# Kernel tuning notes

Measured on AMD Instinct MI355X. Metric: run time of the kernel, lower is better.

The kernel has to match this reference:

```python
import jax, jax.numpy as jnp
import numpy as np

N_NODES = 32768
NUM_EDGES = 524288
NUM_GRAPHS = 32
C = 128            # hidden channels
N_LAYERS = 3       # len(hidden_channels)-1
D_IN = 144         # 4 (op embedding dim) + 140
C_MID = 80         # mem1 out
C_OUT = 64         # mem2 out / classes
H1, K1N = 5, 10    # mem1 heads / clusters
H2, K2N = 5, 1     # mem2 heads / clusters
EPS = 1e-15


def _gatv2(x, src, dst, Wl, bl, Wr, br, att, cb):
    """GATv2Conv (heads=1, negative_slope=0.2), edges src->dst incl. self loops."""
    n = x.shape[0]
    xl = x @ Wl + bl                                  # source transform [N,C]
    xr = x @ Wr + br                                  # target transform [N,C]
    e = (jax.nn.leaky_relu(xl[src] + xr[dst], 0.2) @ att)  # [E]
    m = jax.ops.segment_max(e, dst, num_segments=n)   # segment softmax over in-edges
    ee = jnp.exp(e - m[dst])
    denom = jax.ops.segment_sum(ee, dst, num_segments=n)
    alpha = ee / denom[dst]
    out = jax.ops.segment_sum(alpha[:, None] * xl[src], dst, num_segments=n)
    return out + cb


def _bn(h, gamma, beta):
    # BatchNorm1d with batch statistics (training-mode forward), eps=1e-5
    mu = h.mean(0)
    var = h.var(0)
    return (h - mu) * jax.lax.rsqrt(var + 1e-5) * gamma + beta


def _mem_pool(xd, Kmem, W):
    # xd [B,N,C], Kmem [H,K,C]; Student-t kernel, tau=1 -> (1+d)^-1
    d = (jnp.sum(xd * xd, -1)[:, :, None, None]
         + jnp.sum(Kmem * Kmem, -1)[None, None]
         - 2.0 * jnp.einsum('bnc,hkc->bnhk', xd, Kmem))  # [B,N,H,K] sq. distances
    S = 1.0 / (1.0 + d)
    S = S / S.sum(-1, keepdims=True)   # normalize over clusters
    S = S.mean(2)                      # average heads -> [B,N,K]
    out = jnp.einsum('bnk,bnc->bkc', S, xd) @ W
    return out, S


def _kl_loss(S):
    S2 = S * S / S.sum(1, keepdims=True)
    den = S2.sum(2, keepdims=True)
    den = jnp.where(S.sum(2, keepdims=True) == 0.0, 1.0, den)
    P = jnp.maximum(S2 / den, EPS)
    Sc = jnp.maximum(S, EPS)
    # KLDivLoss(reduction='batchmean'), input = log(S)
    return jnp.sum(P * (jnp.log(P) - jnp.log(Sc))) / S.shape[0]


def setup_inputs():
    key = jax.random.key(0)
    ks = jax.random.split(key, 24)
    x = jax.random.normal(ks[0], (N_NODES, D_IN), jnp.float32)
    edge_index = jax.random.randint(ks[1], (2, NUM_EDGES), 0, N_NODES, jnp.int32)
    batch = (jnp.arange(N_NODES, dtype=jnp.int32) // (N_NODES // NUM_GRAPHS))
    s = 1.0 / np.sqrt(C)
    inp = {
        'x': x, 'edge_index': edge_index, 'batch': batch,
        'W_in': jax.random.normal(ks[2], (D_IN, C), jnp.float32) / np.sqrt(D_IN),
        'b_in': jnp.zeros((C,), jnp.float32),
        'bn_gamma': jnp.ones((N_LAYERS, C), jnp.float32),
        'bn_beta': jnp.zeros((N_LAYERS, C), jnp.float32),
        'Wl': jax.random.normal(ks[3], (N_LAYERS, C, C), jnp.float32) * s,
        'bl': jnp.zeros((N_LAYERS, C), jnp.float32),
        'Wr': jax.random.normal(ks[4], (N_LAYERS, C, C), jnp.float32) * s,
        'br': jnp.zeros((N_LAYERS, C), jnp.float32),
        'att': jax.random.normal(ks[5], (N_LAYERS, C), jnp.float32) * s,
        'conv_bias': jnp.zeros((N_LAYERS, C), jnp.float32),
        'K1': jax.random.normal(ks[6], (H1, K1N, C), jnp.float32),
        'Wm1': jax.random.normal(ks[7], (C, C_MID), jnp.float32) * s,
        'K2': jax.random.normal(ks[8], (H2, K2N, C_MID), jnp.float32),
        'Wm2': jax.random.normal(ks[9], (C_MID, C_OUT), jnp.float32) / np.sqrt(C_MID),
    }
    return inp


def reference(x, edge_index, batch, W_in, b_in, bn_gamma, bn_beta,
              Wl, bl, Wr, br, att, conv_bias, K1, Wm1, K2, Wm2):
    h = x @ W_in + b_in                               # self.linear
    loops = jnp.arange(N_NODES, dtype=edge_index.dtype)
    src = jnp.concatenate([edge_index[0], loops])     # GATv2 add_self_loops=True
    dst = jnp.concatenate([edge_index[1], loops])
    for l in range(N_LAYERS):                         # DeepGCNLayer block='res+'
        t = _bn(h, bn_gamma[l], bn_beta[l])
        t = jax.nn.leaky_relu(t, 0.01)
        # dropout: identity (deterministic reference)
        t = _gatv2(t, src, dst, Wl[l], bl[l], Wr[l], br[l], att[l], conv_bias[l])
        h = h + t
    per = N_NODES // NUM_GRAPHS
    xd = h.reshape(NUM_GRAPHS, per, C)                # to_dense_batch (equal-size graphs)
    x1, S1 = _mem_pool(xd, K1, Wm1)                   # [B,10,80]
    x1 = jax.nn.leaky_relu(x1, 0.01)
    x2, S2 = _mem_pool(x1, K2, Wm2)                   # [B,1,64]
    logits = jax.nn.log_softmax(x2.squeeze(1), -1)    # [B,64]
    return logits, _kl_loss(S1) + _kl_loss(S2)
```

## Files before the change

### kernel.cpp

```cpp
#include <hip/hip_runtime.h>
#include <math.h>

#define N_NODES   32768
#define NUM_EDGES 524288
#define NUM_GRAPHS 32
#define PER_G     1024
#define C         128
#define D_IN      144
#define C_MID     80
#define C_OUT     64
#define NL        3
#define NBINS     32

#define WS_H    0
#define WS_XL   16777216
#define WS_XR   25165824
#define WS_CSR  33554432
#define WS_DEG  35651584
#define WS_CUR  35782656
#define WS_PART 35913728
#define WS_CS   35946496
#define WS_KL   35947776
#define WS_ZERO_BASE WS_DEG
#define WS_ZERO_SIZE (35947780 - 35651584)
#define WS_SC   35948544
#define WS_SH   35949056
#define WS_S1   35949568
#define WS_PP   37260288
#define WS_X1   42503168
#define WS_OFF  42605568
#define WS_WINT 42736640
#define WS_WLRT 42777600

using short8 = __attribute__((ext_vector_type(8))) short;
using f32x4  = __attribute__((ext_vector_type(4))) float;

__device__ __forceinline__ float wave_sum(float v) {
  #pragma unroll
  for (int m = 1; m < 64; m <<= 1) v += __shfl_xor(v, m, 64);
  return v;
}

__device__ __forceinline__ float lrelu2(float v) { return fmaxf(v, 0.2f * v); }

__device__ __forceinline__ unsigned short f2bf(float f) {
  union { float f; unsigned u; } c; c.f = f;
  unsigned r = (c.u + 0x7FFFu + ((c.u >> 16) & 1u)) >> 16;
  return (unsigned short)r;
}
__device__ __forceinline__ float bflo(unsigned u) {
  union { unsigned u; float f; } c; c.u = u << 16; return c.f;
}
__device__ __forceinline__ float bfhi(unsigned u) {
  union { unsigned u; float f; } c; c.u = u & 0xFFFF0000u; return c.f;
}

__global__ void k_count(const int* __restrict__ dst, int* __restrict__ deg) {
  int e = blockIdx.x * 256 + threadIdx.x;
  if (e < NUM_EDGES) atomicAdd(&deg[dst[e]], 1);
}

__global__ __launch_bounds__(1024) void k_scan(const int* __restrict__ deg, int* __restrict__ off) {
  __shared__ int part[1024];
  int t = threadIdx.x;
  int base = t * 32;
  int4 d[8];
  const int4* dp = (const int4*)(deg + base);
  #pragma unroll
  for (int i = 0; i < 8; i++) d[i] = dp[i];
  int s = 0;
  #pragma unroll
  for (int i = 0; i < 8; i++) s += d[i].x + d[i].y + d[i].z + d[i].w;
  part[t] = s;
  __syncthreads();
  for (int dd = 1; dd < 1024; dd <<= 1) {
    int v = (t >= dd) ? part[t - dd] : 0;
    __syncthreads();
    part[t] += v;
    __syncthreads();
  }
  int run = (t == 0) ? 0 : part[t - 1];
  int4* op = (int4*)(off + base);
  #pragma unroll
  for (int i = 0; i < 8; i++) {
    int4 o;
    o.x = run; run += d[i].x;
    o.y = run; run += d[i].y;
    o.z = run; run += d[i].z;
    o.w = run; run += d[i].w;
    op[i] = o;
  }
}

__global__ void k_fill(const int* __restrict__ src, const int* __restrict__ dst,
                       const int* __restrict__ off, int* __restrict__ cur,
                       int* __restrict__ csr) {
  int e = blockIdx.x * 256 + threadIdx.x;
  if (e < NUM_EDGES) {
    int d = dst[e];
    int p = atomicAdd(&cur[d], 1);
    csr[off[d] + p] = src[e];
  }
}

__global__ __launch_bounds__(256) void k_prep(const float* __restrict__ W_in,
    const float* __restrict__ Wl, const float* __restrict__ Wr,
    char* __restrict__ winT, char* __restrict__ wlrT) {
  int bid = blockIdx.x;
  int tid = threadIdx.x;
  int col = tid & 127, hh = tid >> 7;
  if (bid < 4) {
    int q = bid;
    float w0[10], w1[10];
    #pragma unroll
    for (int i = 0; i < 10; i++) {
      int p = 2 * (q * 10 + i) + hh;
      w0[i] = (2 * p < D_IN) ? W_in[(size_t)(2 * p) * C + col] : 0.f;
      w1[i] = (2 * p + 1 < D_IN) ? W_in[(size_t)(2 * p + 1) * C + col] : 0.f;
    }
    #pragma unroll
    for (int i = 0; i < 10; i++) {
      int p = 2 * (q * 10 + i) + hh;
      unsigned pkv = ((unsigned)f2bf(w1[i]) << 16) | f2bf(w0[i]);
      int byte = col * 320 + ((4 * p) ^ (((col >> 1) & 3) << 4));
      *(unsigned*)(winT + byte) = pkv;
    }
  } else {
    int id = bid - 4;
    int m = id >> 2;
    int q = id & 3;
    int l = m >> 1, r = m & 1;
    const float* W = (r ? Wr : Wl) + (size_t)l * C * C;
    char* dst = wlrT + (size_t)m * 32768;
    float w0[8], w1[8];
    #pragma unroll
    for (int i = 0; i < 8; i++) {
      int p = 2 * (q * 8 + i) + hh;
      w0[i] = W[(size_t)(2 * p) * C + col];
      w1[i] = W[(size_t)(2 * p + 1) * C + col];
    }
    #pragma unroll
    for (int i = 0; i < 8; i++) {
      int p = 2 * (q * 8 + i) + hh;
      unsigned pkv = ((unsigned)f2bf(w1[i]) << 16) | f2bf(w0[i]);
      int byte = col * 256 + ((4 * p) ^ ((col & 7) << 4));
      *(unsigned*)(dst + byte) = pkv;
    }
  }
}

__global__ __launch_bounds__(256) void k_lin_mfma(const float* __restrict__ x,
    const char* __restrict__ winT, const float* __restrict__ bias,
    float* __restrict__ h, float* __restrict__ part) {
  __shared__ __align__(16) char smem[61440];
  __shared__ float lsum[128];
  __shared__ float lsum2[128];
  char* tA = smem;
  char* tB = smem + 20480;
  int n0 = blockIdx.x * 64;
  int tid = threadIdx.x;
  if (tid < 128) { lsum[tid] = 0.f; lsum2[tid] = 0.f; }
  {
    float4 xv[10];
    #pragma unroll
    for (int k = 0; k < 10; k++) {
      int idx = k * 256 + tid;
      int row = idx / 40, j = idx - row * 40;
      xv[k] = (j < 36) ? *(const float4*)&x[(size_t)(n0 + row) * D_IN + 4 * j]
                       : (float4){0.f, 0.f, 0.f, 0.f};
    }
    #pragma unroll
    for (int k = 0; k < 10; k++) {
      int idx = k * 256 + tid;
      int row = idx / 40, j = idx - row * 40;
      uint2 pk;
      pk.x = ((unsigned)f2bf(xv[k].y) << 16) | f2bf(xv[k].x);
      pk.y = ((unsigned)f2bf(xv[k].w) << 16) | f2bf(xv[k].z);
      int byte = row * 320 + ((8 * j) ^ (((row >> 1) & 3) << 4));
      *(uint2*)(tA + byte) = pk;
    }
  }
  {
    const uint4* src = (const uint4*)winT;
    uint4* d = (uint4*)tB;
    uint4 v[10];
    #pragma unroll
    for (int k = 0; k < 10; k++) v[k] = src[k * 256 + tid];
    #pragma unroll
    for (int k = 0; k < 10; k++) d[k * 256 + tid] = v[k];
  }
  __syncthreads();
  int l = tid & 63, w = tid >> 6;
  f32x4 acc[8];
  #pragma unroll
  for (int f = 0; f < 8; f++) acc[f] = (f32x4){0.f, 0.f, 0.f, 0.f};
  int arow = w * 16 + (l & 15);
  #pragma unroll
  for (int ks = 0; ks < 5; ks++) {
    int kb = ks * 64 + (l >> 4) * 16;
    short8 a = *(const short8*)(tA + arow * 320 + (kb ^ (((arow >> 1) & 3) << 4)));
    #pragma unroll
    for (int f = 0; f < 8; f++) {
      int col = f * 16 + (l & 15);
      short8 b = *(const short8*)(tB + col * 320 + (kb ^ (((col >> 1) & 3) << 4)));
      acc[f] = __builtin_amdgcn_mfma_f32_16x16x32_bf16(a, b, acc[f], 0, 0, 0);
    }
  }
  int rowb = n0 + w * 16 + (l >> 4) * 4;
  #pragma unroll
  for (int f = 0; f < 8; f++) {
    int col = f * 16 + (l & 15);
    float bv = bias[col];
    float s = 0.f, s2 = 0.f;
    #pragma unroll
    for (int r = 0; r < 4; r++) {
      float v = acc[f][r] + bv;
      h[(size_t)(rowb + r) * C + col] = v;
      s += v; s2 += v * v;
    }
    s  += __shfl_xor(s, 16, 64);  s  += __shfl_xor(s, 32, 64);
    s2 += __shfl_xor(s2, 16, 64); s2 += __shfl_xor(s2, 32, 64);
    if (l < 16) {
      atomicAdd(&lsum[col], s);
      atomicAdd(&lsum2[col], s2);
    }
  }
  __syncthreads();
  if (tid < 128) {
    int bin = blockIdx.x & (NBINS - 1);
    atomicAdd(&part[bin * 256 + tid], lsum[tid]);
    atomicAdd(&part[bin * 256 + 128 + tid], lsum2[tid]);
  }
}

__global__ __launch_bounds__(128) void k_bn_part(const float* __restrict__ h, float* __restrict__ part) {
  int b = blockIdx.x; int c = threadIdx.x;
  float s = 0.f, s2 = 0.f;
  int r0 = b * 64;
  for (int r = 0; r < 64; r++) {
    float v = h[(size_t)(r0 + r) * C + c];
    s += v; s2 += v * v;
  }
  int bin = b & (NBINS - 1);
  atomicAdd(&part[bin * 256 + c], s);
  atomicAdd(&part[bin * 256 + 128 + c], s2);
}

__global__ __launch_bounds__(256) void k_bn_fin(float* __restrict__ part,
    const float* __restrict__ gamma, const float* __restrict__ beta,
    float* __restrict__ sc, float* __restrict__ sh) {
  int tid = threadIdx.x;
  if (tid < 128) {
    double S = 0.0, S2 = 0.0;
    for (int b = 0; b < NBINS; b++) {
      S += (double)part[b * 256 + tid];
      S2 += (double)part[b * 256 + 128 + tid];
    }
    double m = S / (double)N_NODES;
    double var = S2 / (double)N_NODES - m * m;
    float rsig = (float)(1.0 / sqrt(var + 1e-5));
    float scv = rsig * gamma[tid];
    sc[tid] = scv;
    sh[tid] = beta[tid] - (float)m * scv;
  }
  __syncthreads();
  for (int i = tid; i < NBINS * 256; i += 256) part[i] = 0.f;
}

__device__ __forceinline__ void gemm_half(const char* tA, const char* tB,
    const float* bias, unsigned short* out, int n0, int tid) {
  int l = tid & 63, w = tid >> 6;
  f32x4 acc[8];
  #pragma unroll
  for (int f = 0; f < 8; f++) acc[f] = (f32x4){0.f, 0.f, 0.f, 0.f};
  int arow = w * 16 + (l & 15);
  #pragma unroll
  for (int ks = 0; ks < 4; ks++) {
    int kb = ks * 64 + (l >> 4) * 16;
    short8 a = *(const short8*)(tA + arow * 256 + (kb ^ ((arow & 7) << 4)));
    #pragma unroll
    for (int f = 0; f < 8; f++) {
      int col = f * 16 + (l & 15);
      short8 b = *(const short8*)(tB + col * 256 + (kb ^ ((col & 7) << 4)));
      acc[f] = __builtin_amdgcn_mfma_f32_16x16x32_bf16(a, b, acc[f], 0, 0, 0);
    }
  }
  int rowb = n0 + w * 16 + (l >> 4) * 4;
  #pragma unroll
  for (int f = 0; f < 8; f++) {
    int col = f * 16 + (l & 15);
    float bv = bias[col];
    #pragma unroll
    for (int r = 0; r < 4; r++)
      out[(size_t)(rowb + r) * C + col] = f2bf(acc[f][r] + bv);
  }
}

__device__ __forceinline__ void copy_B(char* tB, const char* __restrict__ WT, int tid) {
  const uint4* src = (const uint4*)WT;
  uint4* d = (uint4*)tB;
  uint4 v[8];
  #pragma unroll
  for (int k = 0; k < 8; k++) v[k] = src[k * 256 + tid];
  #pragma unroll
  for (int k = 0; k < 8; k++) d[k * 256 + tid] = v[k];
}

__global__ __launch_bounds__(256) void k_gemm_mfma(const float* __restrict__ h,
    const float* __restrict__ sc, const float* __restrict__ sh,
    const char* __restrict__ WlT, const float* __restrict__ bl,
    const char* __restrict__ WrT, const float* __restrict__ br,
    unsigned short* __restrict__ xl, unsigned short* __restrict__ xr) {
  __shared__ __align__(16) char smem[49152];
  char* tA = smem;
  char* tB = smem + 16384;
  int n0 = blockIdx.x * 64;
  int tid = threadIdx.x;
  {
    int cp = tid & 63, w4 = tid >> 6;
    float2 scv = *(const float2*)&sc[2 * cp];
    float2 shv = *(const float2*)&sh[2 * cp];
    float2 hv[16];
    #pragma unroll
    for (int t = 0; t < 16; t++)
      hv[t] = *(const float2*)&h[(size_t)(n0 + t * 4 + w4) * C + 2 * cp];
    #pragma unroll
    for (int t = 0; t < 16; t++) {
      int node = t * 4 + w4;
      float t0 = hv[t].x * scv.x + shv.x; t0 = fmaxf(t0, 0.01f * t0);
      float t1 = hv[t].y * scv.y + shv.y; t1 = fmaxf(t1, 0.01f * t1);
      unsigned pkv = ((unsigned)f2bf(t1) << 16) | f2bf(t0);
      int byte = node * 256 + ((4 * cp) ^ ((node & 7) << 4));
      *(unsigned*)(tA + byte) = pkv;
    }
  }
  copy_B(tB, WlT, tid);
  __syncthreads();
  gemm_half(tA, tB, bl, xl, n0, tid);
  __syncthreads();
  copy_B(tB, WrT, tid);
  __syncthreads();
  gemm_half(tA, tB, br, xr, n0, tid);
}

#define GAT_EDGE(te, ya, yb, yc, yd)                                       \
  if ((te) > m + 8.f) {                                                    \
    float f_ = __expf(m - (te));                                           \
    ssum = fmaf(ssum, f_, 1.f);                                            \
    acc0 = fmaf(acc0, f_, (ya)); acc1 = fmaf(acc1, f_, (yb));              \
    acc2 = fmaf(acc2, f_, (yc)); acc3 = fmaf(acc3, f_, (yd));              \
    m = (te);                                                              \
  } else {                                                                 \
    float p_ = __expf((te) - m);                                           \
    ssum += p_;                                                            \
    acc0 = fmaf(p_, (ya), acc0); acc1 = fmaf(p_, (yb), acc1);              \
    acc2 = fmaf(p_, (yc), acc2); acc3 = fmaf(p_, (yd), acc3);              \
  }

__global__ __launch_bounds__(256) void k_gat(float* __restrict__ h,
    const unsigned* __restrict__ xlb, const unsigned* __restrict__ xrb,
    const float* __restrict__ att, const float* __restrict__ cb,
    const int* __restrict__ off, const int* __restrict__ deg,
    const int* __restrict__ csr) {
  int tid = threadIdx.x;
  int lane = tid & 63;
  int w = tid >> 6;
  int half = lane >> 5;
  int q = lane & 31;
  int node = blockIdx.x * 8 + w * 2 + half;
  float4 a = *(const float4*)&att[q * 4];
  uint2 ur = *(const uint2*)&xrb[(size_t)node * 64 + q * 2];
  float xr0 = bflo(ur.x), xr1 = bfhi(ur.x), xr2 = bflo(ur.y), xr3 = bfhi(ur.y);
  uint2 us = *(const uint2*)&xlb[(size_t)node * 64 + q * 2];
  float acc0 = bflo(us.x), acc1 = bfhi(us.x), acc2 = bflo(us.y), acc3 = bfhi(us.y);
  float p0 = lrelu2(acc0 + xr0) * a.x + lrelu2(acc1 + xr1) * a.y
           + lrelu2(acc2 + xr2) * a.z + lrelu2(acc3 + xr3) * a.w;
  #pragma unroll
  for (int mm = 1; mm < 32; mm <<= 1) p0 += __shfl_xor(p0, mm, 64);
  float m = p0;
  float ssum = 1.f;
  int o = off[node], dg = deg[node];
  int dgmax = max(dg, __shfl_xor(dg, 32, 64));
  for (int base = 0; base < dgmax; base += 32) {
    int cv = (q < dg - base) ? csr[o + base + q] : 0;
    int nb = min(dgmax - base, 32);
    for (int j = 0; j < nb; j += 4) {
      int s0 = __shfl(cv, (half << 5) + j + 0, 64);
      int s1 = __shfl(cv, (half << 5) + j + 1, 64);
      int s2 = __shfl(cv, (half << 5) + j + 2, 64);
      int s3 = __shfl(cv, (half << 5) + j + 3, 64);
      uint2 u0 = *(const uint2*)&xlb[(size_t)s0 * 64 + q * 2];
      uint2 u1 = *(const uint2*)&xlb[(size_t)s1 * 64 + q * 2];
      uint2 u2 = *(const uint2*)&xlb[(size_t)s2 * 64 + q * 2];
      uint2 u3 = *(const uint2*)&xlb[(size_t)s3 * 64 + q * 2];
      float y00 = bflo(u0.x), y01 = bfhi(u0.x), y02 = bflo(u0.y), y03 = bfhi(u0.y);
      float y10 = bflo(u1.x), y11 = bfhi(u1.x), y12 = bflo(u1.y), y13 = bfhi(u1.y);
      float y20 = bflo(u2.x), y21 = bfhi(u2.x), y22 = bflo(u2.y), y23 = bfhi(u2.y);
      float y30 = bflo(u3.x), y31 = bfhi(u3.x), y32 = bflo(u3.y), y33 = bfhi(u3.y);
      float t0 = lrelu2(y00 + xr0) * a.x + lrelu2(y01 + xr1) * a.y
               + lrelu2(y02 + xr2) * a.z + lrelu2(y03 + xr3) * a.w;
      float t1 = lrelu2(y10 + xr0) * a.x + lrelu2(y11 + xr1) * a.y
               + lrelu2(y12 + xr2) * a.z + lrelu2(y13 + xr3) * a.w;
      float t2 = lrelu2(y20 + xr0) * a.x + lrelu2(y21 + xr1) * a.y
               + lrelu2(y22 + xr2) * a.z + lrelu2(y23 + xr3) * a.w;
      float t3 = lrelu2(y30 + xr0) * a.x + lrelu2(y31 + xr1) * a.y
               + lrelu2(y32 + xr2) * a.z + lrelu2(y33 + xr3) * a.w;
      #pragma unroll
      for (int mm = 1; mm < 32; mm <<= 1) {
        t0 += __shfl_xor(t0, mm, 64);
        t1 += __shfl_xor(t1, mm, 64);
        t2 += __shfl_xor(t2, mm, 64);
        t3 += __shfl_xor(t3, mm, 64);
      }
      int jb = base + j;
      t0 = (jb + 0 < dg) ? t0 : -1e30f;
      t1 = (jb + 1 < dg) ? t1 : -1e30f;
      t2 = (jb + 2 < dg) ? t2 : -1e30f;
      t3 = (jb + 3 < dg) ? t3 : -1e30f;
      GAT_EDGE(t0, y00, y01, y02, y03);
      GAT_EDGE(t1, y10, y11, y12, y13);
      GAT_EDGE(t2, y20, y21, y22, y23);
      GAT_EDGE(t3, y30, y31, y32, y33);
    }
  }
  float inv = 1.f / ssum;
  float4 cbv = *(const float4*)&cb[q * 4];
  float4 hv = *(float4*)&h[(size_t)node * C + q * 4];
  hv.x += acc0 * inv + cbv.x;
  hv.y += acc1 * inv + cbv.y;
  hv.z += acc2 * inv + cbv.z;
  hv.w += acc3 * inv + cbv.w;
  *(float4*)&h[(size_t)node * C + q * 4] = hv;
}

__global__ __launch_bounds__(320) void k_mem1(const float* __restrict__ h,
    const float* __restrict__ K1, float* __restrict__ S1, float* __restrict__ colsum) {
  __shared__ float dd[64 * 51];
  __shared__ float kn[50];
  int tid = threadIdx.x;
  int lane = tid & 63;
  int w = tid >> 6;
  int n0 = blockIdx.x * 64;
  if (tid < 50) {
    const float4* kr = reinterpret_cast<const float4*>(K1 + tid * C);
    float s = 0.f;
    for (int q = 0; q < 32; q++) {
      float4 kv = kr[q];
      s += kv.x * kv.x + kv.y * kv.y + kv.z * kv.z + kv.w * kv.w;
    }
    kn[tid] = s;
  }
  int wu = __builtin_amdgcn_readfirstlane(w);
  const float4* x4 = reinterpret_cast<const float4*>(h + (size_t)(n0 + lane) * C);
  const float4* K4 = reinterpret_cast<const float4*>(K1);
  float acc[10];
  #pragma unroll
  for (int it = 0; it < 10; it++) acc[it] = 0.f;
  float xn = 0.f;
  for (int q = 0; q < 32; q += 2) {
    float4 xa = x4[q], xb = x4[q + 1];
    xn += xa.x * xa.x + xa.y * xa.y + xa.z * xa.z + xa.w * xa.w
        + xb.x * xb.x + xb.y * xb.y + xb.z * xb.z + xb.w * xb.w;
    #pragma unroll
    for (int it = 0; it < 10; it++) {
      int j = wu + 5 * it;
      float4 ka = K4[j * 32 + q], kb = K4[j * 32 + q + 1];
      acc[it] += xa.x * ka.x + xa.y * ka.y + xa.z * ka.z + xa.w * ka.w
               + xb.x * kb.x + xb.y * kb.y + xb.z * kb.z + xb.w * kb.w;
    }
  }
  #pragma unroll
  for (int it = 0; it < 10; it++) dd[lane * 51 + wu + 5 * it] = acc[it];
  __syncthreads();
  if (tid < 64) {
    float sn[10];
    #pragma unroll
    for (int k = 0; k < 10; k++) sn[k] = 0.f;
    #pragma unroll
    for (int hd = 0; hd < 5; hd++) {
      float sh_[10]; float hs = 0.f;
      #pragma unroll
      for (int k = 0; k < 10; k++) {
        int j = hd * 10 + k;
        float dist = xn + kn[j] - 2.f * dd[tid * 51 + j];
        float s = 1.f / (1.f + dist);
        sh_[k] = s; hs += s;
      }
      float inv = 1.f / hs;
      #pragma unroll
      for (int k = 0; k < 10; k++) sn[k] += sh_[k] * inv;
    }
    int b = n0 >> 10;
    #pragma unroll
    for (int k = 0; k < 10; k++) {
      float v = 0.2f * sn[k];
      S1[(n0 + tid) * 10 + k] = v;
      float vs = wave_sum(v);
      if (tid == 0) atomicAdd(&colsum[b * 10 + k], vs);
    }
  }
}

__global__ __launch_bounds__(128) void k_pool1a(const float* __restrict__ h,
    const float* __restrict__ S1, float* __restrict__ pp) {
  int b = blockIdx.x >> 5, ch = blockIdx.x & 31;
  int c = threadIdx.x;
  float acc[10];
  #pragma unroll
  for (int k = 0; k < 10; k++) acc[k] = 0.f;
  int n0 = ch * 32;
  for (int n = 0; n < 32; n++) {
    int i = b * PER_G + n0 + n;
    float xv = h[(size_t)i * C + c];
    #pragma unroll
    for (int k = 0; k < 10; k++) acc[k] += S1[i * 10 + k] * xv;
  }
  #pragma unroll
  for (int k = 0; k < 10; k++) pp[(size_t)((b * 32 + ch) * 10 + k) * C + c] = acc[k];
}

__global__ __launch_bounds__(128) void k_pool1b(const float* __restrict__ pp,
    const float* __restrict__ Wm1, float* __restrict__ x1) {
  int bk = blockIdx.x; int b = bk / 10; int k = bk - b * 10;
  int c = threadIdx.x;
  __shared__ float red[C];
  float r = 0.f;
  for (int ch = 0; ch < 32; ch++) r += pp[(size_t)((b * 32 + ch) * 10 + k) * C + c];
  red[c] = r;
  __syncthreads();
  if (c < C_MID) {
    float o = 0.f;
    for (int mIdx = 0; mIdx < C; mIdx++) o += red[mIdx] * Wm1[mIdx * C_MID + c];
    o = fmaxf(o, 0.01f * o);
    x1[bk * C_MID + c] = o;
  }
}

__global__ __launch_bounds__(256) void k_kl1(const float* __restrict__ S1,
    const float* __restrict__ colsum, float* __restrict__ kl) {
  int i = blockIdx.x * 256 + threadIdx.x;
  int b = i >> 10;
  float s[10], q[10];
  float den = 0.f;
  #pragma unroll
  for (int k = 0; k < 10; k++) {
    s[k] = S1[i * 10 + k];
    q[k] = s[k] * s[k] / colsum[b * 10 + k];
    den += q[k];
  }
  float inv = 1.f / den;
  float term = 0.f;
  #pragma unroll
  for (int k = 0; k < 10; k++) {
    float P = fmaxf(q[k] * inv, 1e-15f);
    float Sc = fmaxf(s[k], 1e-15f);
    term += P * (logf(P) - logf(Sc));
  }
  term *= (1.f / (float)NUM_GRAPHS);
  term = wave_sum(term);
  if ((threadIdx.x & 63) == 0) atomicAdd(kl, term);
}

__global__ __launch_bounds__(128) void k_mem2(const float* __restrict__ x1,
    const float* __restrict__ Wm2, const float* __restrict__ kl, float* __restrict__ out) {
  int b = blockIdx.x;
  __shared__ float t80[C_MID];
  int tid = threadIdx.x;
  if (tid < C_MID) {
    float s = 0.f;
    #pragma unroll
    for (int k = 0; k < 10; k++) s += x1[(b * 10 + k) * C_MID + tid];
    t80[tid] = s;
  }
  __syncthreads();
  if (tid < C_OUT) {
    float o = 0.f;
    for (int mIdx = 0; mIdx < C_MID; mIdx++) o += t80[mIdx] * Wm2[mIdx * C_OUT + tid];
    float mx = o;
    #pragma unroll
    for (int d = 1; d < 64; d <<= 1) mx = fmaxf(mx, __shfl_xor(mx, d, 64));
    float p = expf(o - mx);
    float sum = p;
    #pragma unroll
    for (int d = 1; d < 64; d <<= 1) sum += __shfl_xor(sum, d, 64);
    out[b * C_OUT + tid] = o - mx - logf(sum);
  }
  if (b == 0 && tid == 127) out[NUM_GRAPHS * C_OUT] = kl[0];
}

extern "C" void kernel_launch(void* const* d_in, const int* in_sizes, int n_in,
                              void* d_out, int out_size, void* d_ws, size_t ws_size,
                              hipStream_t stream) {
  const float* x    = (const float*)d_in[0];
  const int*   ei   = (const int*)d_in[1];
  const float* W_in = (const float*)d_in[3];
  const float* b_in = (const float*)d_in[4];
  const float* bn_g = (const float*)d_in[5];
  const float* bn_b = (const float*)d_in[6];
  const float* Wl   = (const float*)d_in[7];
  const float* bl   = (const float*)d_in[8];
  const float* Wr   = (const float*)d_in[9];
  const float* br   = (const float*)d_in[10];
  const float* att  = (const float*)d_in[11];
  const float* cb   = (const float*)d_in[12];
  const float* K1   = (const float*)d_in[13];
  const float* Wm1  = (const float*)d_in[14];
  const float* Wm2  = (const float*)d_in[16];
  float* out = (float*)d_out;

  char* ws = (char*)d_ws;
  float* h    = (float*)(ws + WS_H);
  unsigned short* xlp = (unsigned short*)(ws + WS_XL);
  unsigned short* xrp = (unsigned short*)(ws + WS_XR);
  int*   csr  = (int*)(ws + WS_CSR);
  int*   deg  = (int*)(ws + WS_DEG);
  int*   off  = (int*)(ws + WS_OFF);
  int*   cur  = (int*)(ws + WS_CUR);
  float* part = (float*)(ws + WS_PART);
  float* scv  = (float*)(ws + WS_SC);
  float* shv  = (float*)(ws + WS_SH);
  float* S1p  = (float*)(ws + WS_S1);
  float* cs   = (float*)(ws + WS_CS);
  float* pp   = (float*)(ws + WS_PP);
  float* x1p  = (float*)(ws + WS_X1);
  float* klp  = (float*)(ws + WS_KL);
  char*  winT = ws + WS_WINT;
  char*  wlrT = ws + WS_WLRT;

  const int* srcp = ei;
  const int* dstp = ei + NUM_EDGES;

  hipMemsetAsync(ws + WS_ZERO_BASE, 0, WS_ZERO_SIZE, stream);

  k_prep<<<28, 256, 0, stream>>>(W_in, Wl, Wr, winT, wlrT);
  k_count<<<NUM_EDGES / 256, 256, 0, stream>>>(dstp, deg);
  k_scan<<<1, 1024, 0, stream>>>(deg, off);
  k_fill<<<NUM_EDGES / 256, 256, 0, stream>>>(srcp, dstp, off, cur, csr);

  k_lin_mfma<<<N_NODES / 64, 256, 0, stream>>>(x, winT, b_in, h, part);

  for (int l = 0; l < NL; l++) {
    if (l > 0) k_bn_part<<<N_NODES / 64, 128, 0, stream>>>(h, part);
    k_bn_fin<<<1, 256, 0, stream>>>(part, bn_g + l * C, bn_b + l * C, scv, shv);
    k_gemm_mfma<<<N_NODES / 64, 256, 0, stream>>>(h, scv, shv,
        wlrT + (size_t)(l * 2) * 32768, bl + l * C,
        wlrT + (size_t)(l * 2 + 1) * 32768, br + l * C,
        xlp, xrp);
    k_gat<<<N_NODES / 8, 256, 0, stream>>>(h, (const unsigned*)xlp, (const unsigned*)xrp,
        att + l * C, cb + l * C, off, deg, csr);
  }

  k_mem1<<<N_NODES / 64, 320, 0, stream>>>(h, K1, S1p, cs);
  k_pool1a<<<NUM_GRAPHS * 32, 128, 0, stream>>>(h, S1p, pp);
  k_pool1b<<<NUM_GRAPHS * 10, 128, 0, stream>>>(pp, Wm1, x1p);
  k_kl1<<<N_NODES / 256, 256, 0, stream>>>(S1p, cs, klp);
  k_mem2<<<NUM_GRAPHS, 128, 0, stream>>>(x1p, Wm2, klp, out);
}
```

Measured before the change: 281.5 us.

## Fuse BN finalize via last-block ticket and fold pooling into mem1

The separate BN partial-sum and finalize kernels for layers 1 and 2 become a single kernel. The last block to arrive, detected with an atomic ticket, computes the scale and shift, clears the partials and resets the ticket. The pool1a pass is folded into k_mem1: each block keeps its h rows and soft assignments in shared memory and writes per-64-node partial pooled sums, so h is not re-read from global memory. This removes two kernel launches and one full read of h, at the cost of more shared memory in k_mem1 (about 36 KB), which may lower occupancy, and a threadfence-plus-ticket serialization at the end of the BN kernel.

```diff
diff --git a/kernel.cpp b/kernel.cpp
--- a/kernel.cpp
+++ b/kernel.cpp
@@ -21,8 +21,9 @@
 #define WS_PART 35913728
 #define WS_CS   35946496
 #define WS_KL   35947776
+#define WS_TK   35947780
 #define WS_ZERO_BASE WS_DEG
-#define WS_ZERO_SIZE (35947780 - 35651584)
+#define WS_ZERO_SIZE (35947784 - 35651584)
 #define WS_SC   35948544
 #define WS_SH   35949056
 #define WS_S1   35949568
@@ -233,19 +234,6 @@
   }
 }
 
-__global__ __launch_bounds__(128) void k_bn_part(const float* __restrict__ h, float* __restrict__ part) {
-  int b = blockIdx.x; int c = threadIdx.x;
-  float s = 0.f, s2 = 0.f;
-  int r0 = b * 64;
-  for (int r = 0; r < 64; r++) {
-    float v = h[(size_t)(r0 + r) * C + c];
-    s += v; s2 += v * v;
-  }
-  int bin = b & (NBINS - 1);
-  atomicAdd(&part[bin * 256 + c], s);
-  atomicAdd(&part[bin * 256 + 128 + c], s2);
-}
-
 __global__ __launch_bounds__(256) void k_bn_fin(float* __restrict__ part,
     const float* __restrict__ gamma, const float* __restrict__ beta,
     float* __restrict__ sc, float* __restrict__ sh) {
@@ -265,6 +253,42 @@
   }
   __syncthreads();
   for (int i = tid; i < NBINS * 256; i += 256) part[i] = 0.f;
+}
+
+__global__ __launch_bounds__(128) void k_bn(const float* __restrict__ h,
+    float* __restrict__ part, const float* __restrict__ gamma,
+    const float* __restrict__ beta, float* __restrict__ sc,
+    float* __restrict__ sh, int* __restrict__ ticket) {
+  int b = blockIdx.x; int c = threadIdx.x;
+  float s = 0.f, s2 = 0.f;
+  int r0 = b * 64;
+  for (int r = 0; r < 64; r++) {
+    float v = h[(size_t)(r0 + r) * C + c];
+    s += v; s2 += v * v;
+  }
+  int bin = b & (NBINS - 1);
+  atomicAdd(&part[bin * 256 + c], s);
+  atomicAdd(&part[bin * 256 + 128 + c], s2);
+  __threadfence();
+  __syncthreads();
+  __shared__ int lastFlag;
+  if (c == 0) lastFlag = (atomicAdd(ticket, 1) == gridDim.x - 1) ? 1 : 0;
+  __syncthreads();
+  if (lastFlag) {
+    double S = 0.0, S2 = 0.0;
+    for (int k = 0; k < NBINS; k++) {
+      S  += (double)atomicAdd(&part[k * 256 + c], 0.f);
+      S2 += (double)atomicAdd(&part[k * 256 + 128 + c], 0.f);
+    }
+    double m = S / (double)N_NODES;
+    double var = S2 / (double)N_NODES - m * m;
+    float rsig = (float)(1.0 / sqrt(var + 1e-5));
+    float scv = rsig * gamma[c];
+    sc[c] = scv;
+    sh[c] = beta[c] - (float)m * scv;
+    for (int i = c; i < NBINS * 256; i += 128) part[i] = 0.f;
+    if (c == 0) *ticket = 0;
+  }
 }
 
 __device__ __forceinline__ void gemm_half(const char* tA, const char* tB,
@@ -434,9 +458,12 @@
 }
 
 __global__ __launch_bounds__(320) void k_mem1(const float* __restrict__ h,
-    const float* __restrict__ K1, float* __restrict__ S1, float* __restrict__ colsum) {
+    const float* __restrict__ K1, float* __restrict__ S1,
+    float* __restrict__ colsum, float* __restrict__ pp) {
   __shared__ float dd[64 * 51];
   __shared__ float kn[50];
+  __shared__ float sb[64 * 10];
+  __shared__ float hs[64 * 129];
   int tid = threadIdx.x;
   int lane = tid & 63;
   int w = tid >> 6;
@@ -459,6 +486,10 @@
   float xn = 0.f;
   for (int q = 0; q < 32; q += 2) {
     float4 xa = x4[q], xb = x4[q + 1];
+    if (wu == 0) {
+      *(float4*)&hs[lane * 129 + 4 * q] = xa;
+      *(float4*)&hs[lane * 129 + 4 * (q + 1)] = xb;
+    }
     xn += xa.x * xa.x + xa.y * xa.y + xa.z * xa.z + xa.w * xa.w
         + xb.x * xb.x + xb.y * xb.y + xb.z * xb.z + xb.w * xb.w;
     #pragma unroll
@@ -478,15 +509,15 @@
     for (int k = 0; k < 10; k++) sn[k] = 0.f;
     #pragma unroll
     for (int hd = 0; hd < 5; hd++) {
-      float sh_[10]; float hs = 0.f;
+      float sh_[10]; float hsum = 0.f;
       #pragma unroll
       for (int k = 0; k < 10; k++) {
         int j = hd * 10 + k;
         float dist = xn + kn[j] - 2.f * dd[tid * 51 + j];
         float s = 1.f / (1.f + dist);
-        sh_[k] = s; hs += s;
+        sh_[k] = s; hsum += s;
       }
-      float inv = 1.f / hs;
+      float inv = 1.f / hsum;
       #pragma unroll
       for (int k = 0; k < 10; k++) sn[k] += sh_[k] * inv;
     }
@@ -495,28 +526,20 @@
     for (int k = 0; k < 10; k++) {
       float v = 0.2f * sn[k];
       S1[(n0 + tid) * 10 + k] = v;
+      sb[tid * 10 + k] = v;
       float vs = wave_sum(v);
       if (tid == 0) atomicAdd(&colsum[b * 10 + k], vs);
     }
   }
-}
-
-__global__ __launch_bounds__(128) void k_pool1a(const float* __restrict__ h,
-    const float* __restrict__ S1, float* __restrict__ pp) {
-  int b = blockIdx.x >> 5, ch = blockIdx.x & 31;
-  int c = threadIdx.x;
-  float acc[10];
-  #pragma unroll
-  for (int k = 0; k < 10; k++) acc[k] = 0.f;
-  int n0 = ch * 32;
-  for (int n = 0; n < 32; n++) {
-    int i = b * PER_G + n0 + n;
-    float xv = h[(size_t)i * C + c];
-    #pragma unroll
-    for (int k = 0; k < 10; k++) acc[k] += S1[i * 10 + k] * xv;
-  }
-  #pragma unroll
-  for (int k = 0; k < 10; k++) pp[(size_t)((b * 32 + ch) * 10 + k) * C + c] = acc[k];
+  __syncthreads();
+  for (int idx = tid; idx < 1280; idx += 320) {
+    int k = idx >> 7, c = idx & 127;
+    float s = 0.f;
+    #pragma unroll 8
+    for (int n = 0; n < 64; n++)
+      s += sb[n * 10 + k] * hs[n * 129 + c];
+    pp[(size_t)blockIdx.x * 1280 + idx] = s;
+  }
 }
 
 __global__ __launch_bounds__(128) void k_pool1b(const float* __restrict__ pp,
@@ -525,7 +548,8 @@
   int c = threadIdx.x;
   __shared__ float red[C];
   float r = 0.f;
-  for (int ch = 0; ch < 32; ch++) r += pp[(size_t)((b * 32 + ch) * 10 + k) * C + c];
+  for (int ch = 0; ch < 16; ch++)
+    r += pp[(size_t)(b * 16 + ch) * 1280 + k * 128 + c];
   red[c] = r;
   __syncthreads();
   if (c < C_MID) {
@@ -624,6 +648,7 @@
   float* pp   = (float*)(ws + WS_PP);
   float* x1p  = (float*)(ws + WS_X1);
   float* klp  = (float*)(ws + WS_KL);
+  int*   tk   = (int*)(ws + WS_TK);
   char*  winT = ws + WS_WINT;
   char*  wlrT = ws + WS_WLRT;
 
@@ -640,8 +665,12 @@
   k_lin_mfma<<<N_NODES / 64, 256, 0, stream>>>(x, winT, b_in, h, part);
 
   for (int l = 0; l < NL; l++) {
-    if (l > 0) k_bn_part<<<N_NODES / 64, 128, 0, stream>>>(h, part);
-    k_bn_fin<<<1, 256, 0, stream>>>(part, bn_g + l * C, bn_b + l * C, scv, shv);
+    if (l == 0) {
+      k_bn_fin<<<1, 256, 0, stream>>>(part, bn_g, bn_b, scv, shv);
+    } else {
+      k_bn<<<N_NODES / 64, 128, 0, stream>>>(h, part, bn_g + l * C, bn_b + l * C,
+                                             scv, shv, tk);
+    }
     k_gemm_mfma<<<N_NODES / 64, 256, 0, stream>>>(h, scv, shv,
         wlrT + (size_t)(l * 2) * 32768, bl + l * C,
         wlrT + (size_t)(l * 2 + 1) * 32768, br + l * C,
@@ -650,8 +679,7 @@
         att + l * C, cb + l * C, off, deg, csr);
   }
 
-  k_mem1<<<N_NODES / 64, 320, 0, stream>>>(h, K1, S1p, cs);
-  k_pool1a<<<NUM_GRAPHS * 32, 128, 0, stream>>>(h, S1p, pp);
+  k_mem1<<<N_NODES / 64, 320, 0, stream>>>(h, K1, S1p, cs, pp);
   k_pool1b<<<NUM_GRAPHS * 10, 128, 0, stream>>>(pp, Wm1, x1p);
   k_kl1<<<N_NODES / 256, 256, 0, stream>>>(S1p, cs, klp);
   k_mem2<<<NUM_GRAPHS, 128, 0, stream>>>(x1p, Wm2, klp, out);
```

After: 310.5 us. +10.3%, slower.
